# Optimization experiments

Hardware: AMD Instinct MI355X
Metric: run time of the kernel (lower is better)

## Reference

```python
import jax, jax.numpy as jnp
import numpy as np

H, C = 4, 32            # heads, hidden_channel
HC = H * C              # 128
IN = 128                # in_channel
N = 50000               # nodes in sampled subgraph
E = 200000              # edges
USER, ITEM = 50000, 50000
UB = 200                # ubias_num == ibias_num
DIST = 501
BATCH = 1024
NEG = 0.2               # leaky_relu negative slope


def setup_inputs() -> dict:
    key = jax.random.key(0)
    keys = iter(jax.random.split(key, 64))

    def nrm(shape):
        return jax.random.normal(next(keys), shape, dtype=jnp.float32) * 0.05

    def ri(shape, hi):
        return jax.random.randint(next(keys), shape, 0, hi, dtype=jnp.int32)

    inp = {
        # int (graph) inputs
        "node_idx": ri((N,), USER + ITEM + 1),
        "edge_index": ri((2, E), N),
        "edge_type": ri((E,), 6),
        "t_offset_0": ri((E,), UB + 2),
        "t_offset_1": ri((E,), UB + 2),
        "dists_0": ri((E,), DIST),
        "dists_1": ri((E,), DIST),
        "center_nid": ri((BATCH,), N),
        # parameters
        "id_emb": nrm((USER + ITEM + 1, IN)),
        "ucenter_att_bias": nrm((UB + 2, HC)),
        "icenter_att_bias": nrm((UB + 2, HC)),
        "trans_att_bias": nrm((UB + 2, HC)),
        "ucenter_emb_bias": nrm((UB + 2, HC)),
        "icenter_emb_bias": nrm((UB + 2, HC)),
        "trans_emb_bias": nrm((UB + 2, HC)),
        "ucenter_att_bias_2": nrm((UB * 4 + 2, HC)),
        "icenter_att_bias_2": nrm((UB * 4 + 2, HC)),
        "trans_att_bias_2": nrm((UB * 4 + 2, HC)),
        "ucenter_emb_bias_2": nrm((UB * 4 + 2, HC)),
        "icenter_emb_bias_2": nrm((UB * 4 + 2, HC)),
        "trans_emb_bias_2": nrm((UB * 4 + 2, HC)),
        "udist_att_bias": nrm((DIST, HC)),
        "idist_att_bias": nrm((DIST, HC)),
        "udist_emb_bias": nrm((DIST, HC)),
        "idist_emb_bias": nrm((DIST, HC)),
        "udist_att_bias_2": nrm((DIST, HC)),
        "idist_att_bias_2": nrm((DIST, HC)),
        "udist_emb_bias_2": nrm((DIST, HC)),
        "idist_emb_bias_2": nrm((DIST, HC)),
        "trans_head": nrm((IN, HC)),
        "rnn_w": nrm((2 * HC, HC)),           # rnn_update Linear (no bias)
        "w1": nrm((HC * 2 + IN, HC)),          # pred_head layer 1
        "b1": jnp.zeros((HC,), jnp.float32),
        "w2": nrm((HC, ITEM)),                 # pred_head layer 2
        "b2": jnp.zeros((ITEM,), jnp.float32),
        # per-layer conv params (src/dst projections + attention vectors)
        "wl0": nrm((IN, HC)), "wr0": nrm((IN, HC)),
        "asrc0": nrm((H, C)), "adst0": nrm((H, C)),
        "wl1": nrm((HC, HC)), "wr1": nrm((HC, HC)),
        "asrc1": nrm((H, C)), "adst1": nrm((H, C)),
    }
    return inp


def reference(node_idx, edge_index, edge_type, t_offset_0, t_offset_1, dists_0,
              dists_1, center_nid, id_emb, ucenter_att_bias, icenter_att_bias,
              trans_att_bias, ucenter_emb_bias, icenter_emb_bias, trans_emb_bias,
              ucenter_att_bias_2, icenter_att_bias_2, trans_att_bias_2,
              ucenter_emb_bias_2, icenter_emb_bias_2, trans_emb_bias_2,
              udist_att_bias, idist_att_bias, udist_emb_bias, idist_emb_bias,
              udist_att_bias_2, idist_att_bias_2, udist_emb_bias_2,
              idist_emb_bias_2, trans_head, rnn_w, w1, b1, w2, b2,
              wl0, wr0, asrc0, adst0, wl1, wr1, asrc1, adst1):
    x = id_emb[node_idx]                       # [N, IN] gather
    src, dst = edge_index[0], edge_index[1]
    is_u = (edge_type == 0)[:, None]           # user-center homo edges
    is_homo = (edge_type < 2)[:, None]
    involved = ((edge_type == 0) | (edge_type == 2) | (edge_type == 3))[:, None]

    def edge_bias(u_tab, i_tab, tr_tab, toff):
        # homo edges: type-0 -> user table, type-1 -> item table; hetero -> trans table
        b = jnp.where(is_u, u_tab[toff], jnp.where(is_homo, i_tab[toff], tr_tab[toff]))
        return b.reshape(-1, H, C)

    def dist_bias(u_tab, i_tab, dists):
        b = jnp.where(is_u, u_tab[dists], i_tab[dists]) * involved
        return b.reshape(-1, H, C)

    att_b = [edge_bias(ucenter_att_bias, icenter_att_bias, trans_att_bias, t_offset_0),
             edge_bias(ucenter_att_bias_2, icenter_att_bias_2, trans_att_bias_2, t_offset_1)]
    emb_b = [edge_bias(ucenter_emb_bias, icenter_emb_bias, trans_emb_bias, t_offset_0),
             edge_bias(ucenter_emb_bias_2, icenter_emb_bias_2, trans_emb_bias_2, t_offset_1)]
    att_d = [dist_bias(udist_att_bias, idist_att_bias, dists_0),
             dist_bias(udist_att_bias_2, idist_att_bias_2, dists_1)]
    emb_d = [dist_bias(udist_emb_bias, idist_emb_bias, dists_0),
             dist_bias(udist_emb_bias_2, idist_emb_bias_2, dists_1)]

    n_nodes = x.shape[0]

    def conv(h, wl, wr, asrc, adst, ab, eb, ad, ed):
        k = (h @ wl).reshape(n_nodes, H, C)
        q = (h @ wr).reshape(n_nodes, H, C)
        msg = k[src] + eb + ed                                   # [E,H,C]
        logit = jax.nn.leaky_relu(
            jnp.einsum('ehc,hc->eh', k[src] + ab + ad, asrc)
            + jnp.einsum('ehc,hc->eh', q[dst], adst), NEG)        # [E,H]
        m = jax.ops.segment_max(logit, dst, num_segments=n_nodes)
        a = jnp.exp(logit - m[dst])
        den = jax.ops.segment_sum(a, dst, num_segments=n_nodes)
        alpha = a / jnp.maximum(den[dst], 1e-16)
        out = jax.ops.segment_sum(alpha[..., None] * msg, dst, num_segments=n_nodes)
        return out.reshape(n_nodes, HC)

    layers = [(wl0, wr0, asrc0, adst0), (wl1, wr1, asrc1, adst1)]
    x_inter = [x]
    cur = x
    for i in range(2):
        last = cur @ trans_head if i == 0 else cur
        wl, wr, asrc, adst = layers[i]
        cur = conv(cur, wl, wr, asrc, adst, att_b[i], emb_b[i], att_d[i], emb_d[i])
        cur = jnp.tanh(jnp.concatenate([cur, last], axis=-1) @ rnn_w)
        x_inter.append(cur)
        if i != 1:
            cur = jax.nn.relu(cur)   # dropout: eval mode -> identity

    feat = jnp.concatenate(x_inter, axis=-1)[center_nid]   # [B, 2*HC+IN]
    hdd = jax.nn.leaky_relu(feat @ w1 + b1, NEG)            # dropout eval -> identity
    logits = hdd @ w2 + b2                                  # [B, ITEM]
    return logits
```

## Files before the change

kernel.cpp:

```cpp
#include <hip/hip_runtime.h>
#include <cstdint>
#include <cstddef>

typedef unsigned short u16;
typedef __attribute__((ext_vector_type(8))) short short8;
typedef __attribute__((ext_vector_type(4))) float f32x4;

#define HC_ 128
#define CAP 32
#define OFF_U0   0
#define OFF_I0   202
#define OFF_T0   404
#define OFF_UD0  606
#define OFF_ID0  1107
#define OFF_U2   1608
#define OFF_I2   2410
#define OFF_T2   3212
#define OFF_UD2  4014
#define OFF_ID2  4515
#define DOT_ROWS 5016

__device__ __forceinline__ float b2f(u16 u) {
  union { unsigned int i; float f; } v; v.i = ((unsigned int)u) << 16; return v.f;
}
__device__ __forceinline__ u16 f2b(float f) {
  union { float f; unsigned int i; } v; v.f = f;
  unsigned int r = v.i + 0x7fffu + ((v.i >> 16) & 1u);
  return (u16)(r >> 16);
}

__global__ __launch_bounds__(256) void prolog_k(
    const int* __restrict__ nidx, const float* __restrict__ emb, u16* __restrict__ x,
    const float* u0, const float* i0, const float* t0, const float* ud0, const float* id0,
    const float* u2, const float* i2, const float* t2, const float* ud2, const float* id2,
    const float* __restrict__ asrc0, const float* __restrict__ asrc1,
    float* __restrict__ dots,
    const float* __restrict__ wr0, const float* __restrict__ adst0,
    const float* __restrict__ wr1, const float* __restrict__ adst1,
    float* __restrict__ wq,
    const float* __restrict__ rnn_w, u16* __restrict__ rnn_wb,
    const float* __restrict__ th, u16* __restrict__ Wt,
    int* __restrict__ cur, float* __restrict__ kdot0, float* __restrict__ kdot1, int Nn)
{
  int b = blockIdx.x, t = threadIdx.x;
  const int nbCur  = (Nn + 255) >> 8;
  const int nbKd   = (Nn * 4 + 255) >> 8;
  const int nbGx   = (Nn * 16 + 255) >> 8;
  const int nbDots = (DOT_ROWS * 4 + 255) >> 8;

  if (b < nbCur) { int i = b * 256 + t; if (i < Nn) cur[i] = 0; return; }
  b -= nbCur;
  if (b < nbKd) {
    int i = b * 256 + t;
    if (i < Nn * 4) { kdot0[i] = 0.f; kdot1[i] = 0.f; }
    return;
  }
  b -= nbKd;
  if (b < nbGx) {
    int i = b * 256 + t;
    int n = i >> 4, c = (i & 15) << 3;
    if (n < Nn) {
      int id = nidx[n];
      const float* s = emb + (size_t)id * HC_ + c;
      u16 tmp[8];
#pragma unroll
      for (int j = 0; j < 8; ++j) tmp[j] = f2b(s[j]);
      *(short8*)(x + (size_t)n * HC_ + c) = *(short8*)tmp;
    }
    return;
  }
  b -= nbGx;
  if (b < nbDots) {
    int i = b * 256 + t;
    if (i < DOT_ROWS * 4) {
      int r = i >> 2, h = i & 3;
      const float* tab; int lr; const float* as;
      if      (r < OFF_I0)  { tab = u0;  lr = r;            as = asrc0; }
      else if (r < OFF_T0)  { tab = i0;  lr = r - OFF_I0;   as = asrc0; }
      else if (r < OFF_UD0) { tab = t0;  lr = r - OFF_T0;   as = asrc0; }
      else if (r < OFF_ID0) { tab = ud0; lr = r - OFF_UD0;  as = asrc0; }
      else if (r < OFF_U2)  { tab = id0; lr = r - OFF_ID0;  as = asrc0; }
      else if (r < OFF_I2)  { tab = u2;  lr = r - OFF_U2;   as = asrc1; }
      else if (r < OFF_T2)  { tab = i2;  lr = r - OFF_I2;   as = asrc1; }
      else if (r < OFF_UD2) { tab = t2;  lr = r - OFF_T2;   as = asrc1; }
      else if (r < OFF_ID2) { tab = ud2; lr = r - OFF_UD2;  as = asrc1; }
      else                  { tab = id2; lr = r - OFF_ID2;  as = asrc1; }
      float s = 0.f;
#pragma unroll
      for (int c = 0; c < 32; ++c)
        s += tab[(size_t)lr * HC_ + h * 32 + c] * as[h * 32 + c];
      dots[i] = s;
    }
    return;
  }
  b -= nbDots;
  if (b < 4) {
    int i = b * 256 + t;
    int layer = i >> 9, k = (i >> 2) & 127, h = i & 3;
    const float* wr = layer ? wr1 : wr0;
    const float* ad = layer ? adst1 : adst0;
    float s = 0.f;
#pragma unroll
    for (int c = 0; c < 32; ++c)
      s += wr[(size_t)k * HC_ + h * 32 + c] * ad[h * 32 + c];
    wq[i] = s;
    return;
  }
  b -= 4;
  if (b < 128) {
    int i = b * 256 + t;
    rnn_wb[i] = f2b(rnn_w[i]);
    return;
  }
  b -= 128;
  {
    int i = b * 256 + t;
    if (i < 16384) {
      int r = i >> 7, c = i & 127;
      float s = 0.f;
#pragma unroll 8
      for (int k = 0; k < 128; ++k)
        s += th[r * 128 + k] * rnn_w[(size_t)(128 + k) * 128 + c];
      Wt[i] = f2b(s);
    }
  }
}

__global__ void fill_k(const int* __restrict__ src, const int* __restrict__ dst,
                       const int* __restrict__ ety,
                       const int* __restrict__ toff0, const int* __restrict__ toff1,
                       const int* __restrict__ dist0, const int* __restrict__ dist1,
                       const float* __restrict__ dots,
                       int* __restrict__ cur,
                       int2* __restrict__ m0a, f32x4* __restrict__ e0a,
                       int2* __restrict__ m1a, f32x4* __restrict__ e1a, int E)
{
  int e = blockIdx.x * blockDim.x + threadIdx.x;
  if (e >= E) return;
  int d = dst[e];
  int slot = atomicAdd(&cur[d], 1);
  if (slot >= CAP) return;
  int s = src[e], ty = ety[e];
  int to0 = toff0[e], to1 = toff1[e], di0 = dist0[e], di1 = dist1[e];
  bool inv = (ty == 0 || ty == 2 || ty == 3);
  int ar0 = (ty == 0) ? (OFF_U0 + to0) : (ty < 2) ? (OFF_I0 + to0) : (OFF_T0 + to0);
  int ar1 = (ty == 0) ? (OFF_U2 + to1) : (ty < 2) ? (OFF_I2 + to1) : (OFF_T2 + to1);
  f32x4 e0 = *(const f32x4*)(dots + (size_t)ar0 * 4);
  f32x4 e1 = *(const f32x4*)(dots + (size_t)ar1 * 4);
  if (inv) {
    int dr0 = ((ty == 0) ? OFF_UD0 : OFF_ID0) + di0;
    int dr1 = ((ty == 0) ? OFF_UD2 : OFF_ID2) + di1;
    e0 += *(const f32x4*)(dots + (size_t)dr0 * 4);
    e1 += *(const f32x4*)(dots + (size_t)dr1 * 4);
  }
  size_t ix = (size_t)d * CAP + slot;
  m0a[ix] = make_int2(s, ty | (to0 << 3) | (di0 << 13));
  m1a[ix] = make_int2(s, ty | (to1 << 3) | (di1 << 13));
  e0a[ix] = e0;
  e1a[ix] = e1;
}

template<int EPI, int RELUA, int KS, int AF32, int OF32, int KQ>
__global__ __launch_bounds__(256) void gemm_k(
    const void* __restrict__ A_, const float* __restrict__ W,
    const float* __restrict__ bias, void* __restrict__ C_,
    const float* __restrict__ asrc, const float* __restrict__ wqt,
    float* __restrict__ kdot, float* __restrict__ qdot, int M, int N)
{
  const int lane = threadIdx.x & 63;
  const int wave = threadIdx.x >> 6;
  const int quad = lane >> 4;
  const int l16  = lane & 15;
  const int n0   = blockIdx.y * 64 + wave * 16;
  if (n0 >= N) return;

  short8 bfrag[KS];
#pragma unroll
  for (int ks = 0; ks < KS; ++ks) {
    short8 bf;
    const int kb = ks * 32 + quad * 8;
#pragma unroll
    for (int j = 0; j < 8; ++j)
      bf[j] = (short)f2b(W[(size_t)(kb + j) * N + n0 + l16]);
    bfrag[ks] = bf;
  }
  float bv = 0.f;
  if (EPI == 2 || EPI == 3) bv = bias[n0 + l16];

  const int mtiles = M >> 4;
  for (int mt = blockIdx.x; mt < mtiles; mt += gridDim.x) {
    f32x4 acc = {0.f, 0.f, 0.f, 0.f};
    float qp[4] = {0.f, 0.f, 0.f, 0.f};
    if (AF32) {
      const float* arow = (const float*)A_ + (size_t)(mt * 16 + l16) * (KS * 32);
#pragma unroll
      for (int ks = 0; ks < KS; ++ks) {
        short8 af;
#pragma unroll
        for (int j = 0; j < 8; ++j) {
          float v = arow[ks * 32 + quad * 8 + j];
          if (RELUA) v = fmaxf(v, 0.f);
          af[j] = (short)f2b(v);
        }
        acc = __builtin_amdgcn_mfma_f32_16x16x32_bf16(af, bfrag[ks], acc, 0, 0, 0);
      }
    } else {
      const u16* arow = (const u16*)A_ + (size_t)(mt * 16 + l16) * (KS * 32);
#pragma unroll
      for (int ks = 0; ks < KS; ++ks) {
        short8 af = *(const short8*)(arow + ks * 32 + quad * 8);
        if (RELUA) {
#pragma unroll
          for (int j = 0; j < 8; ++j) af[j] = (af[j] < (short)0) ? (short)0 : af[j];
        }
        if (KQ) {
#pragma unroll
          for (int j = 0; j < 8; ++j) {
            float v = b2f((u16)af[j]);
            const float* wr = wqt + (size_t)(ks * 32 + quad * 8 + j) * 4;
            qp[0] += v * wr[0]; qp[1] += v * wr[1];
            qp[2] += v * wr[2]; qp[3] += v * wr[3];
          }
        }
        acc = __builtin_amdgcn_mfma_f32_16x16x32_bf16(af, bfrag[ks], acc, 0, 0, 0);
      }
    }

    if (KQ) {
#pragma unroll
      for (int h = 0; h < 4; ++h) {
        qp[h] += __shfl_xor(qp[h], 16, 64);
        qp[h] += __shfl_xor(qp[h], 32, 64);
      }
      if (blockIdx.y == 0 && quad == 0) {
        f32x4 qv; qv[0] = qp[0]; qv[1] = qp[1]; qv[2] = qp[2]; qv[3] = qp[3];
        *(f32x4*)(qdot + (size_t)(mt * 16 + l16) * 4) = qv;
      }
      const int hh = n0 >> 5;
      const float asv = asrc[n0 + l16];
#pragma unroll
      for (int r = 0; r < 4; ++r) {
        float sr = acc[r] * asv;
        sr += __shfl_xor(sr, 1, 64); sr += __shfl_xor(sr, 2, 64);
        sr += __shfl_xor(sr, 4, 64); sr += __shfl_xor(sr, 8, 64);
        if (l16 == 0)
          atomicAdd(&kdot[(size_t)(mt * 16 + quad * 4 + r) * 4 + hh], sr);
      }
    }

#pragma unroll
    for (int r = 0; r < 4; ++r) {
      float v = acc[r];
      if (EPI == 2)      { v += bv; v = (v > 0.f) ? v : 0.2f * v; }
      else if (EPI == 3) { v += bv; }
      const size_t idx = (size_t)(mt * 16 + quad * 4 + r) * N + n0 + l16;
      if (OF32) ((float*)C_)[idx] = v;
      else      ((u16*)C_)[idx] = f2b(v);
    }
  }
}

__global__ __launch_bounds__(256) void gemm2_k(
    const float* __restrict__ A1, const u16* __restrict__ W1,
    const u16* __restrict__ A2, const u16* __restrict__ W2,
    u16* __restrict__ Cout, int M)
{
  const int lane = threadIdx.x & 63;
  const int wave = threadIdx.x >> 6;
  const int quad = lane >> 4;
  const int l16  = lane & 15;
  const int n0   = blockIdx.y * 64 + wave * 16;

  short8 bf1[4], bf2[4];
#pragma unroll
  for (int ks = 0; ks < 4; ++ks) {
    short8 a, b;
    const int kb = ks * 32 + quad * 8;
#pragma unroll
    for (int j = 0; j < 8; ++j) {
      a[j] = (short)W1[(size_t)(kb + j) * HC_ + n0 + l16];
      b[j] = (short)W2[(size_t)(kb + j) * HC_ + n0 + l16];
    }
    bf1[ks] = a; bf2[ks] = b;
  }

  const int mtiles = M >> 4;
  for (int mt = blockIdx.x; mt < mtiles; mt += gridDim.x) {
    const int rowm = mt * 16 + l16;
    const float* a1 = A1 + (size_t)rowm * HC_;
    const u16*   a2 = A2 + (size_t)rowm * HC_;
    f32x4 acc = {0.f, 0.f, 0.f, 0.f};
#pragma unroll
    for (int ks = 0; ks < 4; ++ks) {
      short8 af;
      const float* p = a1 + ks * 32 + quad * 8;
#pragma unroll
      for (int j = 0; j < 8; ++j) af[j] = (short)f2b(p[j]);
      acc = __builtin_amdgcn_mfma_f32_16x16x32_bf16(af, bf1[ks], acc, 0, 0, 0);
    }
#pragma unroll
    for (int ks = 0; ks < 4; ++ks) {
      short8 af = *(const short8*)(a2 + ks * 32 + quad * 8);
      acc = __builtin_amdgcn_mfma_f32_16x16x32_bf16(af, bf2[ks], acc, 0, 0, 0);
    }
#pragma unroll
    for (int r = 0; r < 4; ++r)
      Cout[(size_t)(mt * 16 + quad * 4 + r) * HC_ + n0 + l16] = f2b(tanhf(acc[r]));
  }
}

template<int MASKED>
__global__ __launch_bounds__(256) void conv_k(
    const int* __restrict__ cur, const int2* __restrict__ meta,
    const f32x4* __restrict__ edot,
    const u16* __restrict__ kbuf,
    const float* __restrict__ kdot, const float* __restrict__ qdot,
    const float* __restrict__ uemb, const float* __restrict__ iemb,
    const float* __restrict__ temb,
    const float* __restrict__ udemb, const float* __restrict__ idemb,
    const int* __restrict__ center, float* __restrict__ CO, int Ncnt)
{
  __shared__ float als[4][CAP][4];
  const int wv = threadIdx.x >> 6;
  int wid = (blockIdx.x * blockDim.x + threadIdx.x) >> 6;
  if (wid >= Ncnt) return;
  const int lane = threadIdx.x & 63;
  const int n = MASKED ? center[wid] : wid;
  int cnt = cur[n]; if (cnt > CAP) cnt = CAP;
  const int h0 = lane >> 5;
  const int h1 = h0 + 2;
  const float q0 = qdot[n * 4 + h0];
  const float q1 = qdot[n * 4 + h1];
  const int2* mb = meta + (size_t)n * CAP;
  const f32x4* eb = edot + (size_t)n * CAP;

  float den0 = 0.f, den1 = 0.f;
  for (int e = 0; e < cnt; ++e) {
    int s = mb[e].x;
    f32x4 ed = eb[e];
    float l0 = kdot[s * 4 + h0] + q0 + ed[h0];
    float l1 = kdot[s * 4 + h1] + q1 + ed[h1];
    l0 = (l0 > 0.f) ? l0 : 0.2f * l0;
    l1 = (l1 > 0.f) ? l1 : 0.2f * l1;
    float a0 = __expf(fminf(l0, 30.f));
    float a1 = __expf(fminf(l1, 30.f));
    den0 += a0; den1 += a1;
    if ((lane & 31) == 0) { als[wv][e][h0] = a0; als[wv][e][h1] = a1; }
  }
  const float r0 = 1.f / fmaxf(den0, 1e-16f);
  const float r1 = 1.f / fmaxf(den1, 1e-16f);

  float acc0 = 0.f, acc1 = 0.f;
  for (int e = 0; e < cnt; ++e) {
    int2 mrec = mb[e];
    int s = mrec.x;
    int ty = mrec.y & 7, to = (mrec.y >> 3) & 1023, di = mrec.y >> 13;
    float al0 = als[wv][e][h0] * r0;
    float al1 = als[wv][e][h1] * r1;

    float m0 = b2f(kbuf[(size_t)s * HC_ + lane]);
    float m1 = b2f(kbuf[(size_t)s * HC_ + 64 + lane]);
    const float* et = (ty == 0) ? uemb : (ty < 2) ? iemb : temb;
    m0 += et[(size_t)to * HC_ + lane];
    m1 += et[(size_t)to * HC_ + 64 + lane];
    if (ty == 0 || ty == 2 || ty == 3) {
      const float* dt = (ty == 0) ? udemb : idemb;
      m0 += dt[(size_t)di * HC_ + lane];
      m1 += dt[(size_t)di * HC_ + 64 + lane];
    }
    acc0 += al0 * m0;
    acc1 += al1 * m1;
  }
  CO[(size_t)n * HC_ + lane]      = acc0;
  CO[(size_t)n * HC_ + 64 + lane] = acc1;
}

__global__ __launch_bounds__(256) void gh_k(
    const float* __restrict__ CO, const u16* __restrict__ rnn_wb,
    const u16* __restrict__ h1, const u16* __restrict__ xb,
    const int* __restrict__ center, const float* __restrict__ w1,
    const float* __restrict__ b1, u16* __restrict__ hdd)
{
  __shared__ u16 h2s[16][136];
  const int t = threadIdx.x;
  const int lane = t & 63, wave = t >> 6, quad = lane >> 4, l16 = lane & 15;
  const int mt = blockIdx.x;
  const int rowm = mt * 16 + l16;
  const int nid = center[rowm];
  const u16* W1 = rnn_wb;
  const u16* W2 = rnn_wb + HC_ * HC_;

#pragma unroll
  for (int half = 0; half < 2; ++half) {
    const int n0 = half * 64 + wave * 16;
    short8 bf1[4], bf2[4];
#pragma unroll
    for (int ks = 0; ks < 4; ++ks) {
      short8 a, b;
      const int kb = ks * 32 + quad * 8;
#pragma unroll
      for (int j = 0; j < 8; ++j) {
        a[j] = (short)W1[(size_t)(kb + j) * HC_ + n0 + l16];
        b[j] = (short)W2[(size_t)(kb + j) * HC_ + n0 + l16];
      }
      bf1[ks] = a; bf2[ks] = b;
    }
    const float* a1 = CO + (size_t)nid * HC_;
    const u16*   a2 = h1 + (size_t)nid * HC_;
    f32x4 acc = {0.f, 0.f, 0.f, 0.f};
#pragma unroll
    for (int ks = 0; ks < 4; ++ks) {
      short8 af;
      const float* p = a1 + ks * 32 + quad * 8;
#pragma unroll
      for (int j = 0; j < 8; ++j) af[j] = (short)f2b(p[j]);
      acc = __builtin_amdgcn_mfma_f32_16x16x32_bf16(af, bf1[ks], acc, 0, 0, 0);
    }
#pragma unroll
    for (int ks = 0; ks < 4; ++ks) {
      short8 af = *(const short8*)(a2 + ks * 32 + quad * 8);
#pragma unroll
      for (int j = 0; j < 8; ++j) af[j] = (af[j] < (short)0) ? (short)0 : af[j];
      acc = __builtin_amdgcn_mfma_f32_16x16x32_bf16(af, bf2[ks], acc, 0, 0, 0);
    }
#pragma unroll
    for (int r = 0; r < 4; ++r)
      h2s[quad * 4 + r][n0 + l16] = f2b(tanhf(acc[r]));
  }
  __syncthreads();

#pragma unroll
  for (int half = 0; half < 2; ++half) {
    const int n0 = half * 64 + wave * 16;
    short8 bfrag[12];
#pragma unroll
    for (int ks = 0; ks < 12; ++ks) {
      short8 bf;
      const int kb = ks * 32 + quad * 8;
#pragma unroll
      for (int j = 0; j < 8; ++j)
        bf[j] = (short)f2b(w1[(size_t)(kb + j) * HC_ + n0 + l16]);
      bfrag[ks] = bf;
    }
    const float bv = b1[n0 + l16];
    f32x4 acc = {0.f, 0.f, 0.f, 0.f};
#pragma unroll
    for (int ks = 0; ks < 12; ++ks) {
      short8 af;
      if (ks < 4)
        af = *(const short8*)(xb + (size_t)nid * HC_ + ks * 32 + quad * 8);
      else if (ks < 8)
        af = *(const short8*)(h1 + (size_t)nid * HC_ + (ks - 4) * 32 + quad * 8);
      else
        af = *(const short8*)(&h2s[l16][(ks - 8) * 32 + quad * 8]);
      acc = __builtin_amdgcn_mfma_f32_16x16x32_bf16(af, bfrag[ks], acc, 0, 0, 0);
    }
#pragma unroll
    for (int r = 0; r < 4; ++r) {
      float v = acc[r] + bv;
      v = (v > 0.f) ? v : 0.2f * v;
      hdd[(size_t)(mt * 16 + quad * 4 + r) * HC_ + n0 + l16] = f2b(v);
    }
  }
}

extern "C" void kernel_launch(void* const* d_in, const int* in_sizes, int n_in,
                              void* d_out, int out_size, void* d_ws, size_t ws_size,
                              hipStream_t stream)
{
  (void)n_in; (void)out_size; (void)ws_size;
  const int* node_idx = (const int*)d_in[0];
  const int* eidx     = (const int*)d_in[1];
  const int* etype    = (const int*)d_in[2];
  const int* toff0    = (const int*)d_in[3];
  const int* toff1    = (const int*)d_in[4];
  const int* dist0    = (const int*)d_in[5];
  const int* dist1    = (const int*)d_in[6];
  const int* center   = (const int*)d_in[7];
  const float* id_emb   = (const float*)d_in[8];
  const float* u_att    = (const float*)d_in[9];
  const float* i_att    = (const float*)d_in[10];
  const float* t_att    = (const float*)d_in[11];
  const float* u_emb    = (const float*)d_in[12];
  const float* i_emb    = (const float*)d_in[13];
  const float* t_emb    = (const float*)d_in[14];
  const float* u_att2   = (const float*)d_in[15];
  const float* i_att2   = (const float*)d_in[16];
  const float* t_att2   = (const float*)d_in[17];
  const float* u_emb2   = (const float*)d_in[18];
  const float* i_emb2   = (const float*)d_in[19];
  const float* t_emb2   = (const float*)d_in[20];
  const float* ud_att   = (const float*)d_in[21];
  const float* id_att   = (const float*)d_in[22];
  const float* ud_emb   = (const float*)d_in[23];
  const float* id_embd  = (const float*)d_in[24];
  const float* ud_att2  = (const float*)d_in[25];
  const float* id_att2  = (const float*)d_in[26];
  const float* ud_emb2  = (const float*)d_in[27];
  const float* id_emb2  = (const float*)d_in[28];
  const float* trans_head = (const float*)d_in[29];
  const float* rnn_w    = (const float*)d_in[30];
  const float* w1       = (const float*)d_in[31];
  const float* b1       = (const float*)d_in[32];
  const float* w2       = (const float*)d_in[33];
  const float* b2       = (const float*)d_in[34];
  const float* wl0      = (const float*)d_in[35];
  const float* wr0      = (const float*)d_in[36];
  const float* asrc0    = (const float*)d_in[37];
  const float* adst0    = (const float*)d_in[38];
  const float* wl1      = (const float*)d_in[39];
  const float* wr1      = (const float*)d_in[40];
  const float* asrc1    = (const float*)d_in[41];
  const float* adst1    = (const float*)d_in[42];

  const int N_    = in_sizes[0];
  const int E_    = in_sizes[2];
  const int B_    = in_sizes[7];
  const int ITEM_ = in_sizes[34];
  const int* esrc = eidx;
  const int* edst = eidx + E_;

  char* ws = (char*)d_ws;
  size_t off = 0;
  auto alloc = [&](size_t bytes) -> char* {
    char* p = ws + off;
    off += (bytes + 255) & ~(size_t)255;
    return p;
  };
  float* CO_b  = (float*)alloc((size_t)N_ * HC_ * 4);
  u16*   k_b   = (u16*)  alloc((size_t)N_ * HC_ * 2);
  u16*   x_b   = (u16*)  alloc((size_t)N_ * HC_ * 2);
  u16*   h1_b  = (u16*)  alloc((size_t)N_ * HC_ * 2);
  float* kdot0 = (float*)alloc((size_t)N_ * 4 * 4);
  float* kdot1 = (float*)alloc((size_t)N_ * 4 * 4);
  float* qdot  = (float*)alloc((size_t)N_ * 4 * 4);
  float* dots  = (float*)alloc((size_t)DOT_ROWS * 4 * 4);
  float* wq    = (float*)alloc(1024 * 4);
  u16*   rnn_wb= (u16*)  alloc(256 * HC_ * 2);
  u16*   Wt    = (u16*)  alloc(HC_ * HC_ * 2);
  u16*   hdd   = (u16*)  alloc((size_t)B_ * HC_ * 2);
  int*   cur   = (int*)  alloc((size_t)N_ * 4);
  int2*  m0a   = (int2*) alloc((size_t)N_ * CAP * 8);
  int2*  m1a   = (int2*) alloc((size_t)N_ * CAP * 8);
  f32x4* e0a   = (f32x4*)alloc((size_t)N_ * CAP * 16);
  f32x4* e1a   = (f32x4*)alloc((size_t)N_ * CAP * 16);

  const int TB = 256;
  auto nb = [&](long long t) { return (int)((t + TB - 1) / TB); };

  const int nbCur  = (N_ + 255) / 256;
  const int nbKd   = (N_ * 4 + 255) / 256;
  const int nbGx   = (N_ * 16 + 255) / 256;
  const int nbDots = (DOT_ROWS * 4 + 255) / 256;
  const int prologBlocks = nbCur + nbKd + nbGx + nbDots + 4 + 128 + 64;
  prolog_k<<<prologBlocks, TB, 0, stream>>>(
      node_idx, id_emb, x_b,
      u_att, i_att, t_att, ud_att, id_att,
      u_att2, i_att2, t_att2, ud_att2, id_att2,
      asrc0, asrc1, dots,
      wr0, adst0, wr1, adst1, wq,
      rnn_w, rnn_wb, trans_head, Wt,
      cur, kdot0, kdot1, N_);

  fill_k<<<nb(E_), TB, 0, stream>>>(esrc, edst, etype, toff0, toff1, dist0, dist1,
                                    dots, cur, m0a, e0a, m1a, e1a, E_);

  gemm_k<0,0,4,0,0,1><<<dim3(640, 2), TB, 0, stream>>>(
      x_b, wl0, nullptr, k_b, asrc0, wq, kdot0, qdot, N_, HC_);

  conv_k<0><<<nb((long long)N_ * 64), TB, 0, stream>>>(
      cur, m0a, e0a, k_b, kdot0, qdot,
      u_emb, i_emb, t_emb, ud_emb, id_embd, nullptr, CO_b, N_);

  gemm2_k<<<dim3(640, 2), TB, 0, stream>>>(CO_b, rnn_wb, x_b, Wt, h1_b, N_);

  gemm_k<0,1,4,0,0,1><<<dim3(640, 2), TB, 0, stream>>>(
      h1_b, wl1, nullptr, k_b, asrc1, wq + 512, kdot1, qdot, N_, HC_);

  conv_k<1><<<nb((long long)B_ * 64), TB, 0, stream>>>(
      cur, m1a, e1a, k_b, kdot1, qdot,
      u_emb2, i_emb2, t_emb2, ud_emb2, id_emb2, center, CO_b, B_);

  gh_k<<<B_ / 16, TB, 0, stream>>>(CO_b, rnn_wb, h1_b, x_b, center, w1, b1, hdd);

  gemm_k<3,0,4,0,1,0><<<dim3(1, (ITEM_ + 63) / 64), TB, 0, stream>>>(
      hdd, w2, b2, d_out, nullptr, nullptr, nullptr, nullptr, B_, ITEM_);
}
```

Before: 679.7 us.

## Add dedicated output GEMM keeping W2 fragments in registers across M tiles

The final hdd@w2 projection gets its own kernel instead of the generic gemm_k instance. Each wave loads a 64-column slab of w2 once, converts it to bf16 MFMA fragments held in registers, and loops over M tiles, with 8 blocks in x splitting the batch. Output is staged through LDS so bias-added results can be written with float4 stores. This aims to cut repeated B-operand loading and make output writes better coalesced, at the cost of higher register pressure. Each column slab is also loaded redundantly by all 8 x-blocks, and the tail-column handling assumes ITEM is a multiple of 4.

```diff
diff --git a/kernel.cpp b/kernel.cpp
--- a/kernel.cpp
+++ b/kernel.cpp
@@ -461,6 +461,72 @@
       v = (v > 0.f) ? v : 0.2f * v;
       hdd[(size_t)(mt * 16 + quad * 4 + r) * HC_ + n0 + l16] = f2b(v);
     }
+  }
+}
+
+__global__ __launch_bounds__(256) void gemm_out_k(
+    const u16* __restrict__ A, const float* __restrict__ W,
+    const float* __restrict__ bias, float* __restrict__ out, int M, int ITEM)
+{
+  __shared__ float lds[4][16][68];
+  const int lane = threadIdx.x & 63;
+  const int wv   = threadIdx.x >> 6;
+  const int quad = lane >> 4;
+  const int l16  = lane & 15;
+  const int nbase = blockIdx.y * 256 + wv * 64;
+
+  short8 bfrag[4][4];
+#pragma unroll
+  for (int nt = 0; nt < 4; ++nt) {
+    const int colc = nbase + nt * 16 + l16;
+    const int col = (colc < ITEM) ? colc : (ITEM - 1);
+#pragma unroll
+    for (int ks = 0; ks < 4; ++ks) {
+      short8 bf;
+      const int kb = ks * 32 + quad * 8;
+#pragma unroll
+      for (int j = 0; j < 8; ++j)
+        bf[j] = (short)f2b(W[(size_t)(kb + j) * ITEM + col]);
+      bfrag[nt][ks] = bf;
+    }
+  }
+  const int c4 = nbase + l16 * 4;
+  const bool wvalid = (c4 + 3) < ITEM;
+  float4 bv = make_float4(0.f, 0.f, 0.f, 0.f);
+  if (wvalid) bv = *(const float4*)(bias + c4);
+
+  const int mtiles = M >> 4;
+  for (int mt = blockIdx.x; mt < mtiles; mt += gridDim.x) {
+    const u16* arow = A + (size_t)(mt * 16 + l16) * HC_;
+    short8 af[4];
+#pragma unroll
+    for (int ks = 0; ks < 4; ++ks)
+      af[ks] = *(const short8*)(arow + ks * 32 + quad * 8);
+    f32x4 acc[4];
+#pragma unroll
+    for (int nt = 0; nt < 4; ++nt) acc[nt] = (f32x4){0.f, 0.f, 0.f, 0.f};
+#pragma unroll
+    for (int nt = 0; nt < 4; ++nt)
+#pragma unroll
+      for (int ks = 0; ks < 4; ++ks)
+        acc[nt] = __builtin_amdgcn_mfma_f32_16x16x32_bf16(af[ks], bfrag[nt][ks],
+                                                          acc[nt], 0, 0, 0);
+#pragma unroll
+    for (int nt = 0; nt < 4; ++nt)
+#pragma unroll
+      for (int r = 0; r < 4; ++r)
+        lds[wv][quad * 4 + r][nt * 16 + l16] = acc[nt][r];
+    __syncthreads();
+    if (wvalid) {
+#pragma unroll
+      for (int i = 0; i < 4; ++i) {
+        const int row = (lane >> 4) + i * 4;
+        float4 v = *(const float4*)(&lds[wv][row][l16 * 4]);
+        v.x += bv.x; v.y += bv.y; v.z += bv.z; v.w += bv.w;
+        *(float4*)(out + (size_t)(mt * 16 + row) * ITEM + c4) = v;
+      }
+    }
+    __syncthreads();
   }
 }
 
@@ -583,6 +649,6 @@
 
   gh_k<<<B_ / 16, TB, 0, stream>>>(CO_b, rnn_wb, h1_b, x_b, center, w1, b1, hdd);
 
-  gemm_k<3,0,4,0,1,0><<<dim3(1, (ITEM_ + 63) / 64), TB, 0, stream>>>(
-      hdd, w2, b2, d_out, nullptr, nullptr, nullptr, nullptr, B_, ITEM_);
-}
+  gemm_out_k<<<dim3(8, (ITEM_ + 255) / 256), TB, 0, stream>>>(
+      hdd, w2, b2, (float*)d_out, B_, ITEM_);
+}
```

Result: faster. 634.8 us (-6.6%).
